# Kernel tuning notes

Hardware: AMD Instinct MI355X
Metric: run time of the kernel (lower is better)

## Reference

```python
import jax, jax.numpy as jnp
import numpy as np

H, C = 8, 16           # heads, per-head channels
NEG_SLOPE = 0.2        # PyG GATConv leaky_relu slope
N_NODES, N_EDGES, F_IN, N_GRAPHS = 50000, 600000, 64, 500


def setup_inputs() -> dict:
    key = jax.random.key(0)
    ks = jax.random.split(key, 24)
    s = 0.1  # weight init scale
    inp = {
        "x": jax.random.normal(ks[0], (N_NODES, F_IN), jnp.float32),
        "edge_index": jax.random.randint(ks[1], (2, N_EDGES), 0, N_NODES, dtype=jnp.int64),
        "batch": jnp.sort(jax.random.randint(ks[2], (N_NODES,), 0, N_GRAPHS, dtype=jnp.int64)),
        "W1": jax.random.normal(ks[3], (F_IN, H * C), jnp.float32) * s,
        "as1": jax.random.normal(ks[4], (H, C), jnp.float32) * s,
        "ad1": jax.random.normal(ks[5], (H, C), jnp.float32) * s,
        "b1": jnp.zeros((H * C,), jnp.float32),
        "W2": jax.random.normal(ks[6], (H * C, H * C), jnp.float32) * s,
        "as2": jax.random.normal(ks[7], (H, C), jnp.float32) * s,
        "ad2": jax.random.normal(ks[8], (H, C), jnp.float32) * s,
        "b2": jnp.zeros((H * C,), jnp.float32),
        "W3": jax.random.normal(ks[9], (H * C, H * C), jnp.float32) * s,
        "as3": jax.random.normal(ks[10], (H, C), jnp.float32) * s,
        "ad3": jax.random.normal(ks[11], (H, C), jnp.float32) * s,
        "b3": jnp.zeros((H * C,), jnp.float32),
        "fc1_w": jax.random.normal(ks[12], (H * C, 10), jnp.float32) * s,
        "fc1_b": jnp.zeros((10,), jnp.float32),
        "fc2_w": jax.random.normal(ks[13], (10, 1), jnp.float32) * s,
        "fc2_b": jnp.zeros((1,), jnp.float32),
    }
    return inp


def gat_layer(x, src, dst, W, att_src, att_dst, bias, n):
    # x: [N, F_in] -> h: [N, H, C]
    h = (x @ W).reshape(n, H, C)
    a_src = jnp.sum(h * att_src, axis=-1)  # [N, H]
    a_dst = jnp.sum(h * att_dst, axis=-1)  # [N, H]
    e = jax.nn.leaky_relu(a_src[src] + a_dst[dst], NEG_SLOPE)  # [E, H]
    # per-destination segment softmax (numerically stable)
    m = jax.ops.segment_max(e, dst, num_segments=n)            # [N, H]
    e = jnp.exp(e - m[dst])
    z = jax.ops.segment_sum(e, dst, num_segments=n)            # [N, H]
    alpha = e / (z[dst] + 1e-16)                               # [E, H]
    out = jax.ops.segment_sum(h[src] * alpha[:, :, None], dst, num_segments=n)  # [N, H, C]
    return out.reshape(n, H * C) + bias


def reference(x, edge_index, batch, W1, as1, ad1, b1, W2, as2, ad2, b2,
              W3, as3, ad3, b3, fc1_w, fc1_b, fc2_w, fc2_b):
    n = x.shape[0]
    # PyG GATConv default add_self_loops=True
    loop = jnp.arange(n, dtype=edge_index.dtype)
    src = jnp.concatenate([edge_index[0], loop])
    dst = jnp.concatenate([edge_index[1], loop])

    x = jax.nn.relu(gat_layer(x, src, dst, W1, as1, ad1, b1, n))
    x = jax.nn.relu(gat_layer(x, src, dst, W2, as2, ad2, b2, n))
    x = jax.nn.relu(gat_layer(x, src, dst, W3, as3, ad3, b3, n))

    # global_mean_pool over graphs
    sums = jax.ops.segment_sum(x, batch, num_segments=N_GRAPHS)          # [G, 128]
    cnts = jax.ops.segment_sum(jnp.ones((n,), x.dtype), batch, num_segments=N_GRAPHS)
    pooled = sums / jnp.maximum(cnts, 1.0)[:, None]

    hdn = jax.nn.relu(pooled @ fc1_w + fc1_b)
    return hdn @ fc2_w + fc2_b  # [G, 1]
```

## Files before the change

kernel.cpp:

```cpp
#include <hip/hip_runtime.h>
#include <hip/hip_bf16.h>

#define H 8
#define C 16
#define HC 128
#define NEG_SLOPE 0.2f

__global__ void init_kernel(int* __restrict__ deg8, int n) {
    int i = blockIdx.x * 256 + threadIdx.x;
    if (i < n) deg8[i] = 0;
}

__global__ void hist8_gptr_kernel(const int* __restrict__ ei, const int* __restrict__ batch,
                                  int* __restrict__ deg8, int* __restrict__ gptr,
                                  int E, int N, int G) {
    int t = blockIdx.x * 256 + threadIdx.x;
    int* dg = deg8 + (size_t)(blockIdx.x & 7) * N;
    int e0 = t * 8;
    if (e0 + 7 < E) {
        int4 d4a = *(const int4*)(ei + E + e0);
        int4 d4b = *(const int4*)(ei + E + e0 + 4);
        atomicAdd(&dg[d4a.x], 1);
        atomicAdd(&dg[d4a.y], 1);
        atomicAdd(&dg[d4a.z], 1);
        atomicAdd(&dg[d4a.w], 1);
        atomicAdd(&dg[d4b.x], 1);
        atomicAdd(&dg[d4b.y], 1);
        atomicAdd(&dg[d4b.z], 1);
        atomicAdd(&dg[d4b.w], 1);
    } else if (e0 < E) {
        for (int j = e0; j < E; ++j) atomicAdd(&dg[ei[E + j]], 1);
    }
    int n0 = t * 8;
    if (n0 < N) {
        int prev = (n0 == 0) ? -1 : batch[n0 - 1];
        for (int j = 0; j < 8 && n0 + j < N; ++j) {
            int i = n0 + j;
            int cur = batch[i];
            if (cur != prev)
                for (int g = prev + 1; g <= cur; ++g) gptr[g] = i;
            if (i == N - 1)
                for (int g = cur + 1; g <= G; ++g) gptr[g] = N;
            prev = cur;
        }
    }
}

__global__ void deg_reduce_kernel(const int* __restrict__ deg8, int* __restrict__ deg, int N) {
    int d = blockIdx.x * 256 + threadIdx.x;
    if (d >= N) return;
    int s = 1;
#pragma unroll
    for (int c = 0; c < 8; ++c) s += deg8[(size_t)c * N + d];
    deg[d] = s;
}

__global__ void scan_blk_kernel(const int* __restrict__ a, int* __restrict__ o,
                                int* __restrict__ p, int n) {
    __shared__ int sh[256];
    int tid = threadIdx.x;
    int base = blockIdx.x * 1024 + tid * 4;
    int4 v = make_int4(0, 0, 0, 0);
    if (base + 3 < n) v = *(const int4*)(a + base);
    else {
        if (base < n)     v.x = a[base];
        if (base + 1 < n) v.y = a[base + 1];
        if (base + 2 < n) v.z = a[base + 2];
        if (base + 3 < n) v.w = a[base + 3];
    }
    v.x = (v.x + 7) & ~7; v.y = (v.y + 7) & ~7;
    v.z = (v.z + 7) & ~7; v.w = (v.w + 7) & ~7;
    if (base >= n)     v.x = 0;
    if (base + 1 >= n) v.y = 0;
    if (base + 2 >= n) v.z = 0;
    if (base + 3 >= n) v.w = 0;
    int s = v.x + v.y + v.z + v.w;
    sh[tid] = s;
    __syncthreads();
    for (int off = 1; off < 256; off <<= 1) {
        int t = (tid >= off) ? sh[tid - off] : 0;
        __syncthreads();
        sh[tid] += t;
        __syncthreads();
    }
    int excl = sh[tid] - s;
    int4 ov;
    ov.x = excl; ov.y = ov.x + v.x; ov.z = ov.y + v.y; ov.w = ov.z + v.z;
    if (base + 3 < n) *(int4*)(o + base) = ov;
    else {
        if (base < n)     o[base] = ov.x;
        if (base + 1 < n) o[base + 1] = ov.y;
        if (base + 2 < n) o[base + 2] = ov.z;
        if (base + 3 < n) o[base + 3] = ov.w;
    }
    if (tid == 255) p[blockIdx.x] = sh[255];
}

__global__ void scan_part_kernel(int* __restrict__ p, int* __restrict__ tot, int nb) {
    __shared__ int sh[256];
    int tid = threadIdx.x;
    int v = (tid < nb) ? p[tid] : 0;
    sh[tid] = v;
    __syncthreads();
    for (int off = 1; off < 256; off <<= 1) {
        int t = (tid >= off) ? sh[tid - off] : 0;
        __syncthreads();
        sh[tid] += t;
        __syncthreads();
    }
    if (tid < nb) p[tid] = sh[tid] - v;
    if (tid == 255) *tot = sh[255];
}

__global__ void scan_add_kernel(int* __restrict__ o, const int* __restrict__ p, int n) {
    int off = p[blockIdx.x];
    int base = blockIdx.x * 1024 + threadIdx.x * 4;
    if (base + 3 < n) {
        int4 v = *(const int4*)(o + base);
        v.x += off; v.y += off; v.z += off; v.w += off;
        *(int4*)(o + base) = v;
    } else {
        if (base < n)     o[base] += off;
        if (base + 1 < n) o[base + 1] += off;
        if (base + 2 < n) o[base + 2] += off;
        if (base + 3 < n) o[base + 3] += off;
    }
}

__global__ void base_fill_kernel(int* __restrict__ deg8 ,
                                 const int* __restrict__ rowptr, int* __restrict__ csr, int N) {
    int d = blockIdx.x * 256 + threadIdx.x;
    if (d >= N) return;
    int base = rowptr[d];
    csr[base] = d;
    int run = base + 1;
    int cnt[8];
#pragma unroll
    for (int c = 0; c < 8; ++c) cnt[c] = deg8[(size_t)c * N + d];
#pragma unroll
    for (int c = 0; c < 8; ++c) { deg8[(size_t)c * N + d] = run; run += cnt[c]; }
    int rend = rowptr[d + 1];
    for (int p = run; p < rend; ++p) csr[p] = N;
    if (d == 0) {
        int tot = rowptr[N];
        for (int k = 0; k < 64; ++k) csr[tot + k] = N;
    }
}

__global__ void scatter8_kernel(const int* __restrict__ ei, int* __restrict__ base8,
                                int* __restrict__ csr, int E, int N) {
    int t = blockIdx.x * 256 + threadIdx.x;
    int* cur = base8 + (size_t)(blockIdx.x & 7) * N;
    int e0 = t * 8;
    if (e0 + 7 < E) {
        int4 s4a = *(const int4*)(ei + e0);
        int4 s4b = *(const int4*)(ei + e0 + 4);
        int4 d4a = *(const int4*)(ei + E + e0);
        int4 d4b = *(const int4*)(ei + E + e0 + 4);
        int p;
        p = atomicAdd(&cur[d4a.x], 1); csr[p] = s4a.x;
        p = atomicAdd(&cur[d4a.y], 1); csr[p] = s4a.y;
        p = atomicAdd(&cur[d4a.z], 1); csr[p] = s4a.z;
        p = atomicAdd(&cur[d4a.w], 1); csr[p] = s4a.w;
        p = atomicAdd(&cur[d4b.x], 1); csr[p] = s4b.x;
        p = atomicAdd(&cur[d4b.y], 1); csr[p] = s4b.y;
        p = atomicAdd(&cur[d4b.z], 1); csr[p] = s4b.z;
        p = atomicAdd(&cur[d4b.w], 1); csr[p] = s4b.w;
    } else if (e0 < E) {
        for (int j = e0; j < E; ++j) {
            int p = atomicAdd(&cur[ei[E + j]], 1);
            csr[p] = ei[j];
        }
    }
}

template <int K>
__global__ void gemm_att_kernel(const float* __restrict__ x, const float* __restrict__ W,
                                const float* __restrict__ as_, const float* __restrict__ ad_,
                                float* __restrict__ h, float* __restrict__ asrc,
                                float* __restrict__ adst, int n) {
    const int ROWS = 64;
    __shared__ float xs[ROWS][HC];
    int tx = threadIdx.x & 31;
    int ty = threadIdx.x >> 5;
    int row0 = blockIdx.x * ROWS;

    if (blockIdx.x == 0) {
        if (threadIdx.x < HC) h[(size_t)n * HC + threadIdx.x] = 0.f;
        if (threadIdx.x < H)  asrc[(size_t)n * H + threadIdx.x] = -INFINITY;
    }

    const int NV = ROWS * K / 4;
    for (int idx = threadIdx.x; idx < NV; idx += 256) {
        int rr = idx / (K / 4), kk = idx % (K / 4);
        int gr = row0 + rr;
        float4 v = (gr < n) ? ((const float4*)(x + (size_t)gr * K))[kk]
                            : make_float4(0.f, 0.f, 0.f, 0.f);
        *(float4*)(&xs[rr][kk * 4]) = v;
    }
    __syncthreads();

    const float* Wc = W + tx * 4;
    float acc[8][4];
#pragma unroll
    for (int r = 0; r < 8; ++r)
#pragma unroll
        for (int c = 0; c < 4; ++c) acc[r][c] = 0.f;

    float4 wv[4], wn[4];
#pragma unroll
    for (int kk = 0; kk < 4; ++kk)
        wv[kk] = *(const float4*)(Wc + (size_t)kk * HC);

    for (int k = 0; k < K; k += 4) {
        if (k + 4 < K) {
#pragma unroll
            for (int kk = 0; kk < 4; ++kk)
                wn[kk] = *(const float4*)(Wc + (size_t)(k + 4 + kk) * HC);
        }
#pragma unroll
        for (int r = 0; r < 8; ++r) {
            float4 xr = *(const float4*)(&xs[ty * 8 + r][k]);
            acc[r][0] = fmaf(xr.x, wv[0].x, acc[r][0]);
            acc[r][1] = fmaf(xr.x, wv[0].y, acc[r][1]);
            acc[r][2] = fmaf(xr.x, wv[0].z, acc[r][2]);
            acc[r][3] = fmaf(xr.x, wv[0].w, acc[r][3]);
            acc[r][0] = fmaf(xr.y, wv[1].x, acc[r][0]);
            acc[r][1] = fmaf(xr.y, wv[1].y, acc[r][1]);
            acc[r][2] = fmaf(xr.y, wv[1].z, acc[r][2]);
            acc[r][3] = fmaf(xr.y, wv[1].w, acc[r][3]);
            acc[r][0] = fmaf(xr.z, wv[2].x, acc[r][0]);
            acc[r][1] = fmaf(xr.z, wv[2].y, acc[r][1]);
            acc[r][2] = fmaf(xr.z, wv[2].z, acc[r][2]);
            acc[r][3] = fmaf(xr.z, wv[2].w, acc[r][3]);
            acc[r][0] = fmaf(xr.w, wv[3].x, acc[r][0]);
            acc[r][1] = fmaf(xr.w, wv[3].y, acc[r][1]);
            acc[r][2] = fmaf(xr.w, wv[3].z, acc[r][2]);
            acc[r][3] = fmaf(xr.w, wv[3].w, acc[r][3]);
        }
#pragma unroll
        for (int kk = 0; kk < 4; ++kk) wv[kk] = wn[kk];
    }
    __syncthreads();
#pragma unroll
    for (int r = 0; r < 8; ++r) {
        float4 o = make_float4(acc[r][0], acc[r][1], acc[r][2], acc[r][3]);
        *(float4*)(&xs[ty * 8 + r][tx * 4]) = o;
        int row = row0 + ty * 8 + r;
        if (row < n) *(float4*)(h + (size_t)row * HC + tx * 4) = o;
    }
    __syncthreads();

#pragma unroll
    for (int rep = 0; rep < 2; ++rep) {
        int pidx = threadIdx.x + rep * 256;
        int row = pidx >> 3;
        int hd = pidx & 7;
        if (row0 + row < n) {
            const float4* hv = (const float4*)&xs[row][hd * 16];
            const float4* sv = (const float4*)(as_ + hd * 16);
            const float4* dv = (const float4*)(ad_ + hd * 16);
            float s = 0.f, d = 0.f;
#pragma unroll
            for (int j = 0; j < 4; ++j) {
                float4 a = hv[j], u = sv[j], v = dv[j];
                s += a.x * u.x + a.y * u.y + a.z * u.z + a.w * u.w;
                d += a.x * v.x + a.y * v.y + a.z * v.z + a.w * v.w;
            }
            asrc[(size_t)(row0 + row) * H + hd] = s;
            adst[(size_t)(row0 + row) * H + hd] = d;
        }
    }
}

__global__ __launch_bounds__(256, 8)
void gat_agg_kernel(const int* __restrict__ rowptr, const int* __restrict__ csr_src,
                    const float* __restrict__ h, const float* __restrict__ asrc,
                    const float* __restrict__ adst, const float* __restrict__ bias,
                    float* __restrict__ out, int N) {
    __shared__ float red[4][3][64];
    int wid = threadIdx.x >> 6;
    int half = wid & 1;
    int dst = blockIdx.x * 2 + (wid >> 1);
    int lane = threadIdx.x & 63;
    int hd = lane >> 3;

    float z = 0.f, a0 = 0.f, a1 = 0.f;
    if (dst < N) {
        int beg = rowptr[dst], end = rowptr[dst + 1];
        int len = end - beg;
        int hl = ((len >> 1) + 7) & ~7;
        int b0 = half ? beg + hl : beg;
        int e0r = half ? end : beg + hl;
        if (b0 < e0r) {
            float ad = adst[(size_t)dst * H + hd];
            const float2* h2 = (const float2*)h;
            int i0, i1, i2, i3, i4, i5, i6, i7;
            float e0, e1, e2, e3, e4, e5, e6, e7;
            float2 v0, v1, v2, v3, v4, v5, v6, v7;
#define LOADI(S, J) i##S = csr_src[(J)];
#define LOADV(S)                                                           \
    { e##S = asrc[(size_t)i##S * H + hd]; v##S = h2[(size_t)i##S * 64 + lane]; }
#define PROCE(S)                                                           \
    {   float e = e##S + ad;                                               \
        e = e > 0.f ? e : NEG_SLOPE * e;                                   \
        float w = __expf(e);                                               \
        z += w;                                                            \
        a0 = fmaf(w, v##S.x, a0);                                          \
        a1 = fmaf(w, v##S.y, a1);                                          \
    }
            LOADI(0, b0)     LOADI(1, b0 + 1) LOADI(2, b0 + 2) LOADI(3, b0 + 3)
            LOADI(4, b0 + 4) LOADI(5, b0 + 5) LOADI(6, b0 + 6) LOADI(7, b0 + 7)
            LOADV(0) LOADV(1) LOADV(2) LOADV(3) LOADV(4) LOADV(5) LOADV(6) LOADV(7)
            LOADI(0, b0 + 8)  LOADI(1, b0 + 9)  LOADI(2, b0 + 10) LOADI(3, b0 + 11)
            LOADI(4, b0 + 12) LOADI(5, b0 + 13) LOADI(6, b0 + 14) LOADI(7, b0 + 15)
            for (int j = b0; j < e0r; j += 8) {
                PROCE(0) LOADV(0)
                PROCE(1) LOADV(1)
                PROCE(2) LOADV(2)
                PROCE(3) LOADV(3)
                PROCE(4) LOADV(4)
                PROCE(5) LOADV(5)
                PROCE(6) LOADV(6)
                PROCE(7) LOADV(7)
                LOADI(0, j + 16) LOADI(1, j + 17) LOADI(2, j + 18) LOADI(3, j + 19)
                LOADI(4, j + 20) LOADI(5, j + 21) LOADI(6, j + 22) LOADI(7, j + 23)
            }
#undef LOADI
#undef LOADV
#undef PROCE
        }
    }
    red[wid][0][lane] = z;
    red[wid][1][lane] = a0;
    red[wid][2][lane] = a1;
    __syncthreads();
    if (half == 0 && dst < N) {
        z  += red[wid + 1][0][lane];
        a0 += red[wid + 1][1][lane];
        a1 += red[wid + 1][2][lane];
        float inv = 1.f / (z + 1e-16f);
        int c2 = lane * 2;
        float r0 = fmaxf(a0 * inv + bias[c2], 0.f);
        float r1 = fmaxf(a1 * inv + bias[c2 + 1], 0.f);
        *(float2*)(out + (size_t)dst * HC + c2) = make_float2(r0, r1);
    }
}

__global__ void pool_mlp_kernel(const float* __restrict__ x, const int* __restrict__ gptr,
                                const float* __restrict__ fc1w, const float* __restrict__ fc1b,
                                const float* __restrict__ fc2w, const float* __restrict__ fc2b,
                                float* __restrict__ out, int G) {
    __shared__ float sp[HC];
    __shared__ float sh[10];
    int g = blockIdx.x;
    int c = threadIdx.x;
    int beg = gptr[g], end = gptr[g + 1];
    float acc = 0.f;
    for (int n = beg; n < end; ++n) acc += x[(size_t)n * HC + c];
    sp[c] = acc / fmaxf((float)(end - beg), 1.f);
    __syncthreads();
    if (c < 10) {
        float s = fc1b[c];
        for (int k = 0; k < HC; ++k) s = fmaf(sp[k], fc1w[k * 10 + c], s);
        sh[c] = fmaxf(s, 0.f);
    }
    __syncthreads();
    if (c == 0) {
        float o = fc2b[0];
#pragma unroll
        for (int j = 0; j < 10; ++j) o = fmaf(sh[j], fc2w[j], o);
        out[g] = o;
    }
}

extern "C" void kernel_launch(void* const* d_in, const int* in_sizes, int n_in,
                              void* d_out, int out_size, void* d_ws, size_t ws_size,
                              hipStream_t stream) {
    const int N = in_sizes[0] / 64;
    const int E = in_sizes[1] / 2;
    const int G = out_size;
    const int CSR_CAP = E + 8 * N + 64;

    const float* x     = (const float*)d_in[0];
    const int*   ei    = (const int*)d_in[1];
    const int*   batch = (const int*)d_in[2];
    const float* W1 = (const float*)d_in[3];
    const float* as1 = (const float*)d_in[4];
    const float* ad1 = (const float*)d_in[5];
    const float* b1 = (const float*)d_in[6];
    const float* W2 = (const float*)d_in[7];
    const float* as2 = (const float*)d_in[8];
    const float* ad2 = (const float*)d_in[9];
    const float* b2 = (const float*)d_in[10];
    const float* W3 = (const float*)d_in[11];
    const float* as3 = (const float*)d_in[12];
    const float* ad3 = (const float*)d_in[13];
    const float* b3 = (const float*)d_in[14];
    const float* fc1w = (const float*)d_in[15];
    const float* fc1b = (const float*)d_in[16];
    const float* fc2w = (const float*)d_in[17];
    const float* fc2b = (const float*)d_in[18];

    float* ws = (float*)d_ws;
    float* h    = ws;
    float* xb0  = h + (size_t)(N + 1) * HC;
    float* xb1  = xb0 + (size_t)N * HC;
    float* asrc = xb1 + (size_t)N * HC;
    float* adst = asrc + (size_t)(N + 1) * H;
    int* ints   = (int*)(adst + (size_t)N * H);
    int* deg8   = ints;
    int* deg    = deg8 + (size_t)8 * N;
    int* rowptr = deg + N;
    int* gptr   = rowptr + N + 16;
    int* partN  = gptr + G + 16;
    int* csr    = partN + 256;

    dim3 blk(256);
    int grid8   = ((E + 7) / 8 + 255) / 256;
    int grid_n  = (N + 255) / 256;
    int grid_agg = (N + 1) / 2;
    int nbN = (N + 1023) / 1024;

    init_kernel<<<(8 * N + 255) / 256, blk, 0, stream>>>(deg8, 8 * N);
    hist8_gptr_kernel<<<grid8, blk, 0, stream>>>(ei, batch, deg8, gptr, E, N, G);
    deg_reduce_kernel<<<grid_n, blk, 0, stream>>>(deg8, deg, N);
    scan_blk_kernel<<<nbN, blk, 0, stream>>>(deg, rowptr, partN, N);
    scan_part_kernel<<<1, blk, 0, stream>>>(partN, rowptr + N, nbN);
    scan_add_kernel<<<nbN, blk, 0, stream>>>(rowptr, partN, N);
    base_fill_kernel<<<grid_n, blk, 0, stream>>>(deg8, rowptr, csr, N);
    scatter8_kernel<<<grid8, blk, 0, stream>>>(ei, deg8, csr, E, N);

    auto run_layer = [&](const float* xin, int K, const float* W, const float* as_,
                         const float* ad_, const float* b, float* out) {
        if (K == 64)
            gemm_att_kernel<64><<<(N + 63) / 64, blk, 0, stream>>>(xin, W, as_, ad_,
                                                                   h, asrc, adst, N);
        else
            gemm_att_kernel<128><<<(N + 63) / 64, blk, 0, stream>>>(xin, W, as_, ad_,
                                                                    h, asrc, adst, N);
        gat_agg_kernel<<<grid_agg, blk, 0, stream>>>(rowptr, csr, h, asrc, adst, b, out, N);
    };

    run_layer(x,   64,  W1, as1, ad1, b1, xb0);
    run_layer(xb0, 128, W2, as2, ad2, b2, xb1);
    run_layer(xb1, 128, W3, as3, ad3, b3, xb0);

    pool_mlp_kernel<<<G, dim3(128), 0, stream>>>(xb0, gptr, fc1w, fc1b, fc2w, fc2b,
                                                 (float*)d_out, G);
}
```

Measured before the change: 371.2 us.

## Fuse degree reduce into scan, stage W in LDS, one wave per node aggregation

Three separate changes. The degree reduction kernel is folded into the block scan, so the per-copy degree counts are summed while they are loaded and one launch plus a global round trip go away. The GEMM now stages W through double-buffered shared memory in 8-row chunks instead of each thread streaming W from global memory. The aggregation kernel drops the split of each node's edge list across two wavefronts and the shared-memory reduction, and uses one wavefront per destination node, which removes a block barrier but lowers parallelism on nodes with many edges.

```diff
diff --git a/kernel.cpp b/kernel.cpp
--- a/kernel.cpp
+++ b/kernel.cpp
@@ -46,27 +46,28 @@
     }
 }
 
-__global__ void deg_reduce_kernel(const int* __restrict__ deg8, int* __restrict__ deg, int N) {
-    int d = blockIdx.x * 256 + threadIdx.x;
-    if (d >= N) return;
-    int s = 1;
-#pragma unroll
-    for (int c = 0; c < 8; ++c) s += deg8[(size_t)c * N + d];
-    deg[d] = s;
-}
-
-__global__ void scan_blk_kernel(const int* __restrict__ a, int* __restrict__ o,
+__global__ void scan_blk_kernel(const int* __restrict__ deg8, int* __restrict__ o,
                                 int* __restrict__ p, int n) {
     __shared__ int sh[256];
     int tid = threadIdx.x;
     int base = blockIdx.x * 1024 + tid * 4;
-    int4 v = make_int4(0, 0, 0, 0);
-    if (base + 3 < n) v = *(const int4*)(a + base);
-    else {
-        if (base < n)     v.x = a[base];
-        if (base + 1 < n) v.y = a[base + 1];
-        if (base + 2 < n) v.z = a[base + 2];
-        if (base + 3 < n) v.w = a[base + 3];
+    int4 v = make_int4(1, 1, 1, 1);
+    if (base + 3 < n) {
+#pragma unroll
+        for (int c = 0; c < 8; ++c) {
+            int4 t4 = *(const int4*)(deg8 + (size_t)c * n + base);
+            v.x += t4.x; v.y += t4.y; v.z += t4.z; v.w += t4.w;
+        }
+    } else {
+        v = make_int4(0, 0, 0, 0);
+        for (int j = 0; j < 4; ++j) {
+            if (base + j < n) {
+                int s = 1;
+#pragma unroll
+                for (int c = 0; c < 8; ++c) s += deg8[(size_t)c * n + base + j];
+                (&v.x)[j] = s;
+            }
+        }
     }
     v.x = (v.x + 7) & ~7; v.y = (v.y + 7) & ~7;
     v.z = (v.z + 7) & ~7; v.w = (v.w + 7) & ~7;
@@ -181,9 +182,12 @@
                                 float* __restrict__ adst, int n) {
     const int ROWS = 64;
     __shared__ float xs[ROWS][HC];
+    __shared__ float wsh[2][8][HC];
     int tx = threadIdx.x & 31;
     int ty = threadIdx.x >> 5;
     int row0 = blockIdx.x * ROWS;
+    int wrow = threadIdx.x >> 5;
+    int wcol = (threadIdx.x & 31) * 4;
 
     if (blockIdx.x == 0) {
         if (threadIdx.x < HC) h[(size_t)n * HC + threadIdx.x] = 0.f;
@@ -198,50 +202,51 @@
                             : make_float4(0.f, 0.f, 0.f, 0.f);
         *(float4*)(&xs[rr][kk * 4]) = v;
     }
-    __syncthreads();
-
-    const float* Wc = W + tx * 4;
+    *(float4*)&wsh[0][wrow][wcol] = *(const float4*)(W + (size_t)wrow * HC + wcol);
+    __syncthreads();
+
     float acc[8][4];
 #pragma unroll
     for (int r = 0; r < 8; ++r)
 #pragma unroll
         for (int c = 0; c < 4; ++c) acc[r][c] = 0.f;
 
-    float4 wv[4], wn[4];
-#pragma unroll
-    for (int kk = 0; kk < 4; ++kk)
-        wv[kk] = *(const float4*)(Wc + (size_t)kk * HC);
-
-    for (int k = 0; k < K; k += 4) {
-        if (k + 4 < K) {
+    const int NCH = K / 8;
+    for (int c = 0; c < NCH; ++c) {
+        int cur = c & 1;
+        if (c + 1 < NCH)
+            *(float4*)&wsh[cur ^ 1][wrow][wcol] =
+                *(const float4*)(W + (size_t)((c + 1) * 8 + wrow) * HC + wcol);
+#pragma unroll
+        for (int k2 = 0; k2 < 2; ++k2) {
+            float4 wv[4];
 #pragma unroll
             for (int kk = 0; kk < 4; ++kk)
-                wn[kk] = *(const float4*)(Wc + (size_t)(k + 4 + kk) * HC);
-        }
-#pragma unroll
-        for (int r = 0; r < 8; ++r) {
-            float4 xr = *(const float4*)(&xs[ty * 8 + r][k]);
-            acc[r][0] = fmaf(xr.x, wv[0].x, acc[r][0]);
-            acc[r][1] = fmaf(xr.x, wv[0].y, acc[r][1]);
-            acc[r][2] = fmaf(xr.x, wv[0].z, acc[r][2]);
-            acc[r][3] = fmaf(xr.x, wv[0].w, acc[r][3]);
-            acc[r][0] = fmaf(xr.y, wv[1].x, acc[r][0]);
-            acc[r][1] = fmaf(xr.y, wv[1].y, acc[r][1]);
-            acc[r][2] = fmaf(xr.y, wv[1].z, acc[r][2]);
-            acc[r][3] = fmaf(xr.y, wv[1].w, acc[r][3]);
-            acc[r][0] = fmaf(xr.z, wv[2].x, acc[r][0]);
-            acc[r][1] = fmaf(xr.z, wv[2].y, acc[r][1]);
-            acc[r][2] = fmaf(xr.z, wv[2].z, acc[r][2]);
-            acc[r][3] = fmaf(xr.z, wv[2].w, acc[r][3]);
-            acc[r][0] = fmaf(xr.w, wv[3].x, acc[r][0]);
-            acc[r][1] = fmaf(xr.w, wv[3].y, acc[r][1]);
-            acc[r][2] = fmaf(xr.w, wv[3].z, acc[r][2]);
-            acc[r][3] = fmaf(xr.w, wv[3].w, acc[r][3]);
-        }
-#pragma unroll
-        for (int kk = 0; kk < 4; ++kk) wv[kk] = wn[kk];
-    }
-    __syncthreads();
+                wv[kk] = *(const float4*)&wsh[cur][k2 * 4 + kk][tx * 4];
+            int kx = c * 8 + k2 * 4;
+#pragma unroll
+            for (int r = 0; r < 8; ++r) {
+                float4 xr = *(const float4*)(&xs[ty * 8 + r][kx]);
+                acc[r][0] = fmaf(xr.x, wv[0].x, acc[r][0]);
+                acc[r][1] = fmaf(xr.x, wv[0].y, acc[r][1]);
+                acc[r][2] = fmaf(xr.x, wv[0].z, acc[r][2]);
+                acc[r][3] = fmaf(xr.x, wv[0].w, acc[r][3]);
+                acc[r][0] = fmaf(xr.y, wv[1].x, acc[r][0]);
+                acc[r][1] = fmaf(xr.y, wv[1].y, acc[r][1]);
+                acc[r][2] = fmaf(xr.y, wv[1].z, acc[r][2]);
+                acc[r][3] = fmaf(xr.y, wv[1].w, acc[r][3]);
+                acc[r][0] = fmaf(xr.z, wv[2].x, acc[r][0]);
+                acc[r][1] = fmaf(xr.z, wv[2].y, acc[r][1]);
+                acc[r][2] = fmaf(xr.z, wv[2].z, acc[r][2]);
+                acc[r][3] = fmaf(xr.z, wv[2].w, acc[r][3]);
+                acc[r][0] = fmaf(xr.w, wv[3].x, acc[r][0]);
+                acc[r][1] = fmaf(xr.w, wv[3].y, acc[r][1]);
+                acc[r][2] = fmaf(xr.w, wv[3].z, acc[r][2]);
+                acc[r][3] = fmaf(xr.w, wv[3].w, acc[r][3]);
+            }
+        }
+        __syncthreads();
+    }
 #pragma unroll
     for (int r = 0; r < 8; ++r) {
         float4 o = make_float4(acc[r][0], acc[r][1], acc[r][2], acc[r][3]);
@@ -273,31 +278,23 @@
     }
 }
 
-__global__ __launch_bounds__(256, 8)
-void gat_agg_kernel(const int* __restrict__ rowptr, const int* __restrict__ csr_src,
-                    const float* __restrict__ h, const float* __restrict__ asrc,
-                    const float* __restrict__ adst, const float* __restrict__ bias,
-                    float* __restrict__ out, int N) {
-    __shared__ float red[4][3][64];
-    int wid = threadIdx.x >> 6;
-    int half = wid & 1;
-    int dst = blockIdx.x * 2 + (wid >> 1);
+__global__ void gat_agg_kernel(const int* __restrict__ rowptr, const int* __restrict__ csr_src,
+                               const float* __restrict__ h, const float* __restrict__ asrc,
+                               const float* __restrict__ adst, const float* __restrict__ bias,
+                               float* __restrict__ out, int N) {
+    int dst = (blockIdx.x * 256 + threadIdx.x) >> 6;
+    if (dst >= N) return;
     int lane = threadIdx.x & 63;
     int hd = lane >> 3;
+    int beg = rowptr[dst], end = rowptr[dst + 1];
+    float ad = adst[(size_t)dst * H + hd];
+    const float2* h2 = (const float2*)h;
 
     float z = 0.f, a0 = 0.f, a1 = 0.f;
-    if (dst < N) {
-        int beg = rowptr[dst], end = rowptr[dst + 1];
-        int len = end - beg;
-        int hl = ((len >> 1) + 7) & ~7;
-        int b0 = half ? beg + hl : beg;
-        int e0r = half ? end : beg + hl;
-        if (b0 < e0r) {
-            float ad = adst[(size_t)dst * H + hd];
-            const float2* h2 = (const float2*)h;
-            int i0, i1, i2, i3, i4, i5, i6, i7;
-            float e0, e1, e2, e3, e4, e5, e6, e7;
-            float2 v0, v1, v2, v3, v4, v5, v6, v7;
+    int i0, i1, i2, i3, i4, i5, i6, i7;
+    float e0, e1, e2, e3, e4, e5, e6, e7;
+    float2 v0, v1, v2, v3, v4, v5, v6, v7;
+
 #define LOADI(S, J) i##S = csr_src[(J)];
 #define LOADV(S)                                                           \
     { e##S = asrc[(size_t)i##S * H + hd]; v##S = h2[(size_t)i##S * 64 + lane]; }
@@ -309,42 +306,32 @@
         a0 = fmaf(w, v##S.x, a0);                                          \
         a1 = fmaf(w, v##S.y, a1);                                          \
     }
-            LOADI(0, b0)     LOADI(1, b0 + 1) LOADI(2, b0 + 2) LOADI(3, b0 + 3)
-            LOADI(4, b0 + 4) LOADI(5, b0 + 5) LOADI(6, b0 + 6) LOADI(7, b0 + 7)
-            LOADV(0) LOADV(1) LOADV(2) LOADV(3) LOADV(4) LOADV(5) LOADV(6) LOADV(7)
-            LOADI(0, b0 + 8)  LOADI(1, b0 + 9)  LOADI(2, b0 + 10) LOADI(3, b0 + 11)
-            LOADI(4, b0 + 12) LOADI(5, b0 + 13) LOADI(6, b0 + 14) LOADI(7, b0 + 15)
-            for (int j = b0; j < e0r; j += 8) {
-                PROCE(0) LOADV(0)
-                PROCE(1) LOADV(1)
-                PROCE(2) LOADV(2)
-                PROCE(3) LOADV(3)
-                PROCE(4) LOADV(4)
-                PROCE(5) LOADV(5)
-                PROCE(6) LOADV(6)
-                PROCE(7) LOADV(7)
-                LOADI(0, j + 16) LOADI(1, j + 17) LOADI(2, j + 18) LOADI(3, j + 19)
-                LOADI(4, j + 20) LOADI(5, j + 21) LOADI(6, j + 22) LOADI(7, j + 23)
-            }
+    LOADI(0, beg)     LOADI(1, beg + 1) LOADI(2, beg + 2) LOADI(3, beg + 3)
+    LOADI(4, beg + 4) LOADI(5, beg + 5) LOADI(6, beg + 6) LOADI(7, beg + 7)
+    LOADV(0) LOADV(1) LOADV(2) LOADV(3) LOADV(4) LOADV(5) LOADV(6) LOADV(7)
+    LOADI(0, beg + 8)  LOADI(1, beg + 9)  LOADI(2, beg + 10) LOADI(3, beg + 11)
+    LOADI(4, beg + 12) LOADI(5, beg + 13) LOADI(6, beg + 14) LOADI(7, beg + 15)
+
+    for (int j = beg; j < end; j += 8) {
+        PROCE(0) LOADV(0)
+        PROCE(1) LOADV(1)
+        PROCE(2) LOADV(2)
+        PROCE(3) LOADV(3)
+        PROCE(4) LOADV(4)
+        PROCE(5) LOADV(5)
+        PROCE(6) LOADV(6)
+        PROCE(7) LOADV(7)
+        LOADI(0, j + 16) LOADI(1, j + 17) LOADI(2, j + 18) LOADI(3, j + 19)
+        LOADI(4, j + 20) LOADI(5, j + 21) LOADI(6, j + 22) LOADI(7, j + 23)
+    }
 #undef LOADI
 #undef LOADV
 #undef PROCE
-        }
-    }
-    red[wid][0][lane] = z;
-    red[wid][1][lane] = a0;
-    red[wid][2][lane] = a1;
-    __syncthreads();
-    if (half == 0 && dst < N) {
-        z  += red[wid + 1][0][lane];
-        a0 += red[wid + 1][1][lane];
-        a1 += red[wid + 1][2][lane];
-        float inv = 1.f / (z + 1e-16f);
-        int c2 = lane * 2;
-        float r0 = fmaxf(a0 * inv + bias[c2], 0.f);
-        float r1 = fmaxf(a1 * inv + bias[c2 + 1], 0.f);
-        *(float2*)(out + (size_t)dst * HC + c2) = make_float2(r0, r1);
-    }
+    float inv = 1.f / (z + 1e-16f);
+    int c2 = lane * 2;
+    float r0 = fmaxf(a0 * inv + bias[c2], 0.f);
+    float r1 = fmaxf(a1 * inv + bias[c2 + 1], 0.f);
+    *(float2*)(out + (size_t)dst * HC + c2) = make_float2(r0, r1);
 }
 
 __global__ void pool_mlp_kernel(const float* __restrict__ x, const int* __restrict__ gptr,
@@ -410,8 +397,7 @@
     float* adst = asrc + (size_t)(N + 1) * H;
     int* ints   = (int*)(adst + (size_t)N * H);
     int* deg8   = ints;
-    int* deg    = deg8 + (size_t)8 * N;
-    int* rowptr = deg + N;
+    int* rowptr = deg8 + (size_t)8 * N;
     int* gptr   = rowptr + N + 16;
     int* partN  = gptr + G + 16;
     int* csr    = partN + 256;
@@ -419,13 +405,12 @@
     dim3 blk(256);
     int grid8   = ((E + 7) / 8 + 255) / 256;
     int grid_n  = (N + 255) / 256;
-    int grid_agg = (N + 1) / 2;
+    int grid_agg = (N * 64 + 255) / 256;
     int nbN = (N + 1023) / 1024;
 
     init_kernel<<<(8 * N + 255) / 256, blk, 0, stream>>>(deg8, 8 * N);
     hist8_gptr_kernel<<<grid8, blk, 0, stream>>>(ei, batch, deg8, gptr, E, N, G);
-    deg_reduce_kernel<<<grid_n, blk, 0, stream>>>(deg8, deg, N);
-    scan_blk_kernel<<<nbN, blk, 0, stream>>>(deg, rowptr, partN, N);
+    scan_blk_kernel<<<nbN, blk, 0, stream>>>(deg8, rowptr, partN, N);
     scan_part_kernel<<<1, blk, 0, stream>>>(partN, rowptr + N, nbN);
     scan_add_kernel<<<nbN, blk, 0, stream>>>(rowptr, partN, N);
     base_fill_kernel<<<grid_n, blk, 0, stream>>>(deg8, rowptr, csr, N);
```

Measured after the change: 362.5 us, median of 2. -2.4%, faster.
